# Optimization experiments

Hardware: AMD Instinct MI355X
Metric: run time of the kernel (lower is better)

## Reference

```python
import jax, jax.numpy as jnp
import numpy as np

NUM_CONTEXT = 8  # context panels; +1 choice -> 9 panels, 72 ordered pairs (i != j)

_PAIRS = np.array([(i, j) for i in range(9) for j in range(9) if i != j], dtype=np.int32)
I_IDX = jnp.asarray(_PAIRS[:, 0])  # [72]
J_IDX = jnp.asarray(_PAIRS[:, 1])  # [72]


def setup_inputs() -> dict:
    key = jax.random.key(0)
    ks = jax.random.split(key, 10)
    B, C, F, H = 256, 8, 512, 256
    s_in = 1.0 / np.sqrt(2 * F)
    s_h = 1.0 / np.sqrt(H)
    return {
        "context_features": jax.random.normal(ks[0], (B, NUM_CONTEXT, F), jnp.float32),
        "choice_features": jax.random.normal(ks[1], (B, C, F), jnp.float32),
        "W1": jax.random.uniform(ks[2], (2 * F, H), jnp.float32, -s_in, s_in),
        "b1": jax.random.uniform(ks[3], (H,), jnp.float32, -s_in, s_in),
        "W2": jax.random.uniform(ks[4], (H, H), jnp.float32, -s_h, s_h),
        "b2": jax.random.uniform(ks[5], (H,), jnp.float32, -s_h, s_h),
        "W3": jax.random.uniform(ks[6], (H, H), jnp.float32, -s_h, s_h),
        "b3": jax.random.uniform(ks[7], (H,), jnp.float32, -s_h, s_h),
        "W4": jax.random.uniform(ks[8], (H, 1), jnp.float32, -s_h, s_h),
        "b4": jax.random.uniform(ks[9], (1,), jnp.float32, -s_h, s_h),
    }


def reference(context_features, choice_features, W1, b1, W2, b2, W3, b3, W4, b4):
    B, C, F = choice_features.shape[0], choice_features.shape[1], choice_features.shape[2]
    # panels[b, c, p, f]: 8 context panels + 1 choice panel per candidate choice
    ctx = jnp.broadcast_to(context_features[:, None, :, :], (B, C, NUM_CONTEXT, F))
    panels = jnp.concatenate([ctx, choice_features[:, :, None, :]], axis=2)  # [B,C,9,F]
    # all 72 ordered pairs (i != j), concatenated features -> [B,C,72,2F]
    pair = jnp.concatenate([panels[:, :, I_IDX, :], panels[:, :, J_IDX, :]], axis=-1)
    # g_theta MLP
    h = jax.nn.relu(pair @ W1 + b1)
    h = jax.nn.relu(h @ W2 + b2)        # [B,C,72,H]
    agg = h.mean(axis=2)                # [B,C,H]
    # f_phi MLP (dropout is identity in eval mode)
    g = jax.nn.relu(agg @ W3 + b3)
    score = g @ W4 + b4                 # [B,C,1]
    return score[..., 0]                # [B,C]
```

## Files before the change

kernel.cpp:

```cpp
#include <hip/hip_runtime.h>
#include <hip/hip_bf16.h>


typedef __bf16 bf16_t;
typedef bf16_t bf16x8 __attribute__((ext_vector_type(8)));
typedef bf16_t bf16x4 __attribute__((ext_vector_type(4)));
typedef float f32x4 __attribute__((ext_vector_type(4)));

#define MFMA16(a, b, c) __builtin_amdgcn_mfma_f32_16x16x32_bf16((a), (b), (c), 0, 0, 0)

__global__ __launch_bounds__(256) void prep_kernel(
    const float* __restrict__ W1, const float* __restrict__ W2,
    const float* __restrict__ W3, bf16_t* __restrict__ Wp,
    bf16_t* __restrict__ W2T, bf16_t* __restrict__ W3T) {
  __shared__ float Ts[64][65];
  const int b = blockIdx.x;
  const int t = threadIdx.x;
  const int r = t >> 6;
  const int c = t & 63;
  const float* srcP;
  bf16_t* dstP;
  int srcRow, srcCol, dr0, dc0, dstride;
  if (b < 64) {
    const int k0 = (b >> 3) * 64, j0 = (b & 7) * 64;
    srcP = W1; dstP = Wp; dstride = 512;
    srcRow = (j0 < 256) ? k0 : 512 + k0;
    srcCol = (j0 < 256) ? j0 : j0 - 256;
    dr0 = j0; dc0 = k0;
  } else if (b < 80) {
    const int s = b - 64;
    const int k0 = (s >> 2) * 64, n0 = (s & 3) * 64;
    srcP = W2; dstP = W2T; dstride = 256;
    srcRow = k0; srcCol = n0; dr0 = n0; dc0 = k0;
  } else {
    const int s = b - 80;
    const int k0 = (s >> 2) * 64, n0 = (s & 3) * 64;
    srcP = W3; dstP = W3T; dstride = 256;
    srcRow = k0; srcCol = n0; dr0 = n0; dc0 = k0;
  }
  for (int i = 0; i < 16; ++i) {
    const int a = i * 4 + r;
    Ts[a][c] = srcP[(size_t)(srcRow + a) * 256 + srcCol + c];
  }
  __syncthreads();
  for (int i = 0; i < 16; ++i) {
    const int j = i * 4 + r;
    dstP[(size_t)(dr0 + j) * dstride + dc0 + c] = (bf16_t)Ts[c][j];
  }
}

__global__ __launch_bounds__(512) void k1_kernel(
    const float* __restrict__ ctx, const float* __restrict__ cho,
    const bf16_t* __restrict__ Wp, bf16_t* __restrict__ UV) {
  __shared__ bf16_t As[64][264];
  const int bm = blockIdx.x & 63;
  const int bn = blockIdx.x >> 6;
  const int t = threadIdx.x;
  const int lane = t & 63;
  const int w = t >> 6;
  const int col = lane & 15;
  const int quad = lane >> 4;
  const int n = bn * 128 + w * 16 + col;
  const int sr = t >> 3;
  const int gr = bm * 64 + sr;
  const int bi = gr >> 4;
  const int p = gr & 15;
  const float* src = (p < 8) ? ctx + (size_t)(bi * 8 + p) * 512
                             : cho + (size_t)(bi * 8 + (p - 8)) * 512;
  const int cb = (t & 7) * 4;
  f32x4 acc[4] = {};
  for (int half = 0; half < 2; ++half) {
    const int kbase = half * 256;
    for (int i = 0; i < 8; ++i) {
      const int c = cb + i * 32;
      const f32x4 x = *(const f32x4*)(src + kbase + c);
      bf16x4 y;
      for (int e = 0; e < 4; ++e) y[e] = (bf16_t)x[e];
      *(bf16x4*)(&As[sr][c]) = y;
    }
    __syncthreads();
    for (int ks = 0; ks < 8; ++ks) {
      const int k = ks * 32 + quad * 8;
      bf16x8 af[4];
      for (int mt = 0; mt < 4; ++mt)
        af[mt] = *(const bf16x8*)(&As[mt * 16 + col][k]);
      const bf16x8 bf = *(const bf16x8*)(Wp + (size_t)n * 512 + kbase + k);
      for (int mt = 0; mt < 4; ++mt) acc[mt] = MFMA16(af[mt], bf, acc[mt]);
    }
    __syncthreads();
  }
  for (int mt = 0; mt < 4; ++mt)
    for (int reg = 0; reg < 4; ++reg) {
      const int r = bm * 64 + mt * 16 + quad * 4 + reg;
      UV[(size_t)r * 512 + n] = (bf16_t)acc[mt][reg];
    }
}

__global__ __launch_bounds__(512) void k2_kernel(
    const bf16_t* __restrict__ UV, const float* __restrict__ b1,
    const float* __restrict__ b2, const bf16_t* __restrict__ W2T,
    const bf16_t* __restrict__ W3T, const float* __restrict__ b3,
    const float* __restrict__ W4, const float* __restrict__ b4,
    float* __restrict__ out) {
  __shared__ char smem[52224];
  bf16_t (*h1)[136] = (bf16_t(*)[136])smem;
  float (*S)[256] = (float(*)[256])smem;
  bf16_t (*Ag)[264] = (bf16_t(*)[264])(smem + 9216);
  float (*red)[8] = (float(*)[8])(smem + 9216 + 8448);
  const int b = blockIdx.x;
  const int t = threadIdx.x;
  const int lane = t & 63;
  const int w = t >> 6;
  const int col = lane & 15;
  const int quad = lane >> 4;
  const bf16_t* su = nullptr;
  const bf16_t* sv = nullptr;
  int sr = 0, sc0 = 0;
  if (t < 384) {
    sr = t >> 1;
    sc0 = (t & 1) * 64;
    if (sr < 56) {
      const int i = sr / 7;
      const int jj = sr - i * 7;
      const int j = jj + (jj >= i ? 1 : 0);
      su = UV + (size_t)(b * 16 + i) * 512;
      sv = UV + (size_t)(b * 16 + j) * 512 + 256;
    } else if (sr >= 64) {
      const int ch = (sr - 64) >> 4;
      const int rr = (sr - 64) & 15;
      if (rr < 8) {
        su = UV + (size_t)(b * 16 + 8 + ch) * 512;
        sv = UV + (size_t)(b * 16 + rr) * 512 + 256;
      } else {
        su = UV + (size_t)(b * 16 + (rr - 8)) * 512;
        sv = UV + (size_t)(b * 16 + 8 + ch) * 512 + 256;
      }
    }
  }
  const int mtb = (w & 1) * 6;
  const int q = w >> 1;
  f32x4 acc[6][4] = {};
  for (int half = 0; half < 2; ++half) {
    const int kbase = half * 128;
    if (t < 384) {
      if (su) {
        for (int c = sc0; c < sc0 + 64; c += 8) {
          const bf16x8 u8 = *(const bf16x8*)(su + kbase + c);
          const bf16x8 v8 = *(const bf16x8*)(sv + kbase + c);
          const f32x4 bb0 = *(const f32x4*)(b1 + kbase + c);
          const f32x4 bb1 = *(const f32x4*)(b1 + kbase + c + 4);
          bf16x8 y;
          for (int e = 0; e < 4; ++e)
            y[e] = (bf16_t)fmaxf((float)u8[e] + (float)v8[e] + bb0[e], 0.0f);
          for (int e = 0; e < 4; ++e)
            y[4 + e] = (bf16_t)fmaxf((float)u8[4 + e] + (float)v8[4 + e] + bb1[e], 0.0f);
          *(bf16x8*)(&h1[sr][c]) = y;
        }
      } else if (half == 0) {
        for (int c = sc0; c < sc0 + 64; c += 8)
          *(bf16x8*)(&h1[sr][c]) = (bf16x8)0.0f;
      }
    }
    __syncthreads();
    for (int ks = 0; ks < 4; ++ks) {
      const int k = ks * 32 + quad * 8;
      bf16x8 af[6], bf[4];
      for (int mt = 0; mt < 6; ++mt)
        af[mt] = *(const bf16x8*)(&h1[(mtb + mt) * 16 + col][k]);
      for (int nt = 0; nt < 4; ++nt) {
        const int n = q * 64 + nt * 16 + col;
        bf[nt] = *(const bf16x8*)(W2T + (size_t)n * 256 + kbase + k);
      }
      for (int mt = 0; mt < 6; ++mt)
        for (int nt = 0; nt < 4; ++nt)
          acc[mt][nt] = MFMA16(af[mt], bf[nt], acc[mt][nt]);
    }
    __syncthreads();
  }
  for (int nt = 0; nt < 4; ++nt) {
    const int n = q * 64 + nt * 16 + col;
    const float b2c = b2[n];
    float sctx = 0.0f;
    for (int mt = 0; mt < 6; ++mt) {
      const int gm = mtb + mt;
      float s = 0.0f;
      for (int reg = 0; reg < 4; ++reg) {
        const int row = gm * 16 + quad * 4 + reg;
        if (row < 56 || row >= 64) s += fmaxf(acc[mt][nt][reg] + b2c, 0.0f);
      }
      s += __shfl_xor(s, 16);
      s += __shfl_xor(s, 32);
      if (gm < 4) {
        sctx += s;
      } else if (lane < 16) {
        S[1 + (gm - 4)][n] = s;
      }
    }
    if (mtb == 0 && lane < 16) S[0][n] = sctx;
  }
  __syncthreads();
  {
    const int ch = t >> 6;
    const int n0 = (t & 63) * 4;
    bf16x4 y;
    for (int e = 0; e < 4; ++e)
      y[e] = (bf16_t)((S[0][n0 + e] + S[1 + ch][n0 + e]) * (1.0f / 72.0f));
    *(bf16x4*)(&Ag[ch][n0]) = y;
    *(bf16x4*)(&Ag[8 + ch][n0]) = (bf16x4)0.0f;
  }
  __syncthreads();
  f32x4 acc2[2] = {};
  for (int ks = 0; ks < 8; ++ks) {
    const int k = ks * 32 + quad * 8;
    const bf16x8 af = *(const bf16x8*)(&Ag[col][k]);
    for (int nt = 0; nt < 2; ++nt) {
      const int n = w * 32 + nt * 16 + col;
      const bf16x8 bf = *(const bf16x8*)(W3T + (size_t)n * 256 + k);
      acc2[nt] = MFMA16(af, bf, acc2[nt]);
    }
  }
  for (int reg = 0; reg < 4; ++reg) {
    float pr = 0.0f;
    for (int nt = 0; nt < 2; ++nt) {
      const int n = w * 32 + nt * 16 + col;
      pr += fmaxf(acc2[nt][reg] + b3[n], 0.0f) * W4[n];
    }
    pr += __shfl_xor(pr, 1);
    pr += __shfl_xor(pr, 2);
    pr += __shfl_xor(pr, 4);
    pr += __shfl_xor(pr, 8);
    if (col == 0 && quad < 2) red[w][quad * 4 + reg] = pr;
  }
  __syncthreads();
  if (t < 8) {
    float sc = b4[0];
    for (int ww = 0; ww < 8; ++ww) sc += red[ww][t];
    out[b * 8 + t] = sc;
  }
}

extern "C" void kernel_launch(void* const* d_in, const int* in_sizes, int n_in,
                              void* d_out, int out_size, void* d_ws, size_t ws_size,
                              hipStream_t stream) {
  (void)in_sizes; (void)n_in; (void)out_size; (void)ws_size;
  const float* ctx = (const float*)d_in[0];
  const float* cho = (const float*)d_in[1];
  const float* W1  = (const float*)d_in[2];
  const float* b1  = (const float*)d_in[3];
  const float* W2  = (const float*)d_in[4];
  const float* b2  = (const float*)d_in[5];
  const float* W3  = (const float*)d_in[6];
  const float* b3  = (const float*)d_in[7];
  const float* W4  = (const float*)d_in[8];
  const float* b4  = (const float*)d_in[9];
  char* ws = (char*)d_ws;
  bf16_t* Wp   = (bf16_t*)(ws + 0);
  bf16_t* W2T  = (bf16_t*)(ws + 524288);
  bf16_t* W3T  = (bf16_t*)(ws + 655360);
  bf16_t* UV   = (bf16_t*)(ws + 786432);
  float*  out  = (float*)d_out;

  prep_kernel<<<dim3(96), dim3(256), 0, stream>>>(W1, W2, W3, Wp, W2T, W3T);
  k1_kernel<<<dim3(256), dim3(512), 0, stream>>>(ctx, cho, Wp, UV);
  k2_kernel<<<dim3(256), dim3(512), 0, stream>>>(UV, b1, b2, W2T, W3T, b3, W4, b4, out);
}
```

Baseline: 109.7 us.

## Fuse first-layer projection into the pair MLP kernel, keeping UV in LDS

Merges the first GEMM kernel (per-panel U/V projections) into the second kernel. Each block now converts its 16 panels to bf16 in shared memory, computes the 16x512 UV tile with MFMA, and builds the pair hidden layer straight from LDS, so the global UV round trip and one launch disappear. The layer-2 GEMM now runs over all of K in one pass instead of two halves, which removes a sync pair. In exchange each block re-reads the full 512x512 Wp weight (256 blocks instead of 64 per column tile), and shared memory grows to about 118KB, allowing only one block per CU.

```diff
diff --git a/kernel.cpp b/kernel.cpp
--- a/kernel.cpp
+++ b/kernel.cpp
@@ -49,134 +49,118 @@
   }
 }
 
-__global__ __launch_bounds__(512) void k1_kernel(
+__global__ __launch_bounds__(512) void k2_kernel(
     const float* __restrict__ ctx, const float* __restrict__ cho,
-    const bf16_t* __restrict__ Wp, bf16_t* __restrict__ UV) {
-  __shared__ bf16_t As[64][264];
-  const int bm = blockIdx.x & 63;
-  const int bn = blockIdx.x >> 6;
-  const int t = threadIdx.x;
-  const int lane = t & 63;
-  const int w = t >> 6;
-  const int col = lane & 15;
-  const int quad = lane >> 4;
-  const int n = bn * 128 + w * 16 + col;
-  const int sr = t >> 3;
-  const int gr = bm * 64 + sr;
-  const int bi = gr >> 4;
-  const int p = gr & 15;
-  const float* src = (p < 8) ? ctx + (size_t)(bi * 8 + p) * 512
-                             : cho + (size_t)(bi * 8 + (p - 8)) * 512;
-  const int cb = (t & 7) * 4;
-  f32x4 acc[4] = {};
-  for (int half = 0; half < 2; ++half) {
-    const int kbase = half * 256;
-    for (int i = 0; i < 8; ++i) {
-      const int c = cb + i * 32;
-      const f32x4 x = *(const f32x4*)(src + kbase + c);
-      bf16x4 y;
-      for (int e = 0; e < 4; ++e) y[e] = (bf16_t)x[e];
-      *(bf16x4*)(&As[sr][c]) = y;
-    }
-    __syncthreads();
-    for (int ks = 0; ks < 8; ++ks) {
-      const int k = ks * 32 + quad * 8;
-      bf16x8 af[4];
-      for (int mt = 0; mt < 4; ++mt)
-        af[mt] = *(const bf16x8*)(&As[mt * 16 + col][k]);
-      const bf16x8 bf = *(const bf16x8*)(Wp + (size_t)n * 512 + kbase + k);
-      for (int mt = 0; mt < 4; ++mt) acc[mt] = MFMA16(af[mt], bf, acc[mt]);
-    }
-    __syncthreads();
-  }
-  for (int mt = 0; mt < 4; ++mt)
-    for (int reg = 0; reg < 4; ++reg) {
-      const int r = bm * 64 + mt * 16 + quad * 4 + reg;
-      UV[(size_t)r * 512 + n] = (bf16_t)acc[mt][reg];
-    }
-}
-
-__global__ __launch_bounds__(512) void k2_kernel(
-    const bf16_t* __restrict__ UV, const float* __restrict__ b1,
+    const bf16_t* __restrict__ Wp, const float* __restrict__ b1,
     const float* __restrict__ b2, const bf16_t* __restrict__ W2T,
     const bf16_t* __restrict__ W3T, const float* __restrict__ b3,
     const float* __restrict__ W4, const float* __restrict__ b4,
     float* __restrict__ out) {
-  __shared__ char smem[52224];
-  bf16_t (*h1)[136] = (bf16_t(*)[136])smem;
-  float (*S)[256] = (float(*)[256])smem;
-  bf16_t (*Ag)[264] = (bf16_t(*)[264])(smem + 9216);
-  float (*red)[8] = (float(*)[8])(smem + 9216 + 8448);
+  __shared__ char smem[118016];
+  bf16_t (*UVs)[520] = (bf16_t(*)[520])smem;
+  bf16_t (*Xs)[520]  = (bf16_t(*)[520])(smem + 16640);
+  bf16_t (*h1)[264]  = (bf16_t(*)[264])(smem + 16640);
+  float  (*S)[256]   = (float(*)[256])(smem + 16640);
+  bf16_t (*Ag)[264]  = (bf16_t(*)[264])(smem + 16640 + 9216);
+  float  (*red)[8]   = (float(*)[8])(smem + 16640 + 9216 + 8448);
   const int b = blockIdx.x;
   const int t = threadIdx.x;
   const int lane = t & 63;
   const int w = t >> 6;
   const int col = lane & 15;
   const int quad = lane >> 4;
-  const bf16_t* su = nullptr;
-  const bf16_t* sv = nullptr;
-  int sr = 0, sc0 = 0;
+
+  {
+    const int row = t >> 5;
+    const int c0 = (t & 31) * 16;
+    const float* src = (row < 8) ? ctx + ((size_t)b * 8 + row) * 512
+                                 : cho + ((size_t)b * 8 + (row - 8)) * 512;
+    const f32x4 x0 = *(const f32x4*)(src + c0);
+    const f32x4 x1 = *(const f32x4*)(src + c0 + 4);
+    const f32x4 x2 = *(const f32x4*)(src + c0 + 8);
+    const f32x4 x3 = *(const f32x4*)(src + c0 + 12);
+    bf16x8 y0, y1;
+    for (int e = 0; e < 4; ++e) { y0[e] = (bf16_t)x0[e]; y0[4 + e] = (bf16_t)x1[e]; }
+    for (int e = 0; e < 4; ++e) { y1[e] = (bf16_t)x2[e]; y1[4 + e] = (bf16_t)x3[e]; }
+    *(bf16x8*)(&Xs[row][c0]) = y0;
+    *(bf16x8*)(&Xs[row][c0 + 8]) = y1;
+  }
+  __syncthreads();
+
+  {
+    f32x4 acc1[4] = {};
+    for (int ks = 0; ks < 16; ++ks) {
+      const int k = ks * 32 + quad * 8;
+      const bf16x8 af = *(const bf16x8*)(&Xs[col][k]);
+      for (int nt = 0; nt < 4; ++nt) {
+        const int n = w * 64 + nt * 16 + col;
+        const bf16x8 bfr = *(const bf16x8*)(Wp + (size_t)n * 512 + k);
+        acc1[nt] = MFMA16(af, bfr, acc1[nt]);
+      }
+    }
+    for (int nt = 0; nt < 4; ++nt) {
+      const int n = w * 64 + nt * 16 + col;
+      for (int reg = 0; reg < 4; ++reg)
+        UVs[quad * 4 + reg][n] = (bf16_t)acc1[nt][reg];
+    }
+  }
+  __syncthreads();
+
   if (t < 384) {
-    sr = t >> 1;
-    sc0 = (t & 1) * 64;
+    const int sr = t >> 1;
+    const int sc0 = (t & 1) * 128;
+    const bf16_t* su = nullptr;
+    const bf16_t* sv = nullptr;
     if (sr < 56) {
       const int i = sr / 7;
       const int jj = sr - i * 7;
       const int j = jj + (jj >= i ? 1 : 0);
-      su = UV + (size_t)(b * 16 + i) * 512;
-      sv = UV + (size_t)(b * 16 + j) * 512 + 256;
+      su = UVs[i];
+      sv = UVs[j] + 256;
     } else if (sr >= 64) {
       const int ch = (sr - 64) >> 4;
       const int rr = (sr - 64) & 15;
-      if (rr < 8) {
-        su = UV + (size_t)(b * 16 + 8 + ch) * 512;
-        sv = UV + (size_t)(b * 16 + rr) * 512 + 256;
-      } else {
-        su = UV + (size_t)(b * 16 + (rr - 8)) * 512;
-        sv = UV + (size_t)(b * 16 + 8 + ch) * 512 + 256;
-      }
-    }
-  }
+      if (rr < 8) { su = UVs[8 + ch]; sv = UVs[rr] + 256; }
+      else        { su = UVs[rr - 8]; sv = UVs[8 + ch] + 256; }
+    }
+    if (su) {
+      for (int c = sc0; c < sc0 + 128; c += 8) {
+        const bf16x8 u8 = *(const bf16x8*)(su + c);
+        const bf16x8 v8 = *(const bf16x8*)(sv + c);
+        const f32x4 bb0 = *(const f32x4*)(b1 + c);
+        const f32x4 bb1 = *(const f32x4*)(b1 + c + 4);
+        bf16x8 y;
+        for (int e = 0; e < 4; ++e)
+          y[e] = (bf16_t)fmaxf((float)u8[e] + (float)v8[e] + bb0[e], 0.0f);
+        for (int e = 0; e < 4; ++e)
+          y[4 + e] = (bf16_t)fmaxf((float)u8[4 + e] + (float)v8[4 + e] + bb1[e], 0.0f);
+        *(bf16x8*)(&h1[sr][c]) = y;
+      }
+    } else {
+      for (int c = sc0; c < sc0 + 128; c += 8)
+        *(bf16x8*)(&h1[sr][c]) = (bf16x8)0.0f;
+    }
+  }
+  __syncthreads();
+
   const int mtb = (w & 1) * 6;
   const int q = w >> 1;
   f32x4 acc[6][4] = {};
-  for (int half = 0; half < 2; ++half) {
-    const int kbase = half * 128;
-    if (t < 384) {
-      if (su) {
-        for (int c = sc0; c < sc0 + 64; c += 8) {
-          const bf16x8 u8 = *(const bf16x8*)(su + kbase + c);
-          const bf16x8 v8 = *(const bf16x8*)(sv + kbase + c);
-          const f32x4 bb0 = *(const f32x4*)(b1 + kbase + c);
-          const f32x4 bb1 = *(const f32x4*)(b1 + kbase + c + 4);
-          bf16x8 y;
-          for (int e = 0; e < 4; ++e)
-            y[e] = (bf16_t)fmaxf((float)u8[e] + (float)v8[e] + bb0[e], 0.0f);
-          for (int e = 0; e < 4; ++e)
-            y[4 + e] = (bf16_t)fmaxf((float)u8[4 + e] + (float)v8[4 + e] + bb1[e], 0.0f);
-          *(bf16x8*)(&h1[sr][c]) = y;
-        }
-      } else if (half == 0) {
-        for (int c = sc0; c < sc0 + 64; c += 8)
-          *(bf16x8*)(&h1[sr][c]) = (bf16x8)0.0f;
-      }
-    }
-    __syncthreads();
-    for (int ks = 0; ks < 4; ++ks) {
-      const int k = ks * 32 + quad * 8;
-      bf16x8 af[6], bf[4];
-      for (int mt = 0; mt < 6; ++mt)
-        af[mt] = *(const bf16x8*)(&h1[(mtb + mt) * 16 + col][k]);
-      for (int nt = 0; nt < 4; ++nt) {
-        const int n = q * 64 + nt * 16 + col;
-        bf[nt] = *(const bf16x8*)(W2T + (size_t)n * 256 + kbase + k);
-      }
-      for (int mt = 0; mt < 6; ++mt)
-        for (int nt = 0; nt < 4; ++nt)
-          acc[mt][nt] = MFMA16(af[mt], bf[nt], acc[mt][nt]);
-    }
-    __syncthreads();
-  }
+  for (int ks = 0; ks < 8; ++ks) {
+    const int k = ks * 32 + quad * 8;
+    bf16x8 af[6], bfr[4];
+    for (int mt = 0; mt < 6; ++mt)
+      af[mt] = *(const bf16x8*)(&h1[(mtb + mt) * 16 + col][k]);
+    for (int nt = 0; nt < 4; ++nt) {
+      const int n = q * 64 + nt * 16 + col;
+      bfr[nt] = *(const bf16x8*)(W2T + (size_t)n * 256 + k);
+    }
+    for (int mt = 0; mt < 6; ++mt)
+      for (int nt = 0; nt < 4; ++nt)
+        acc[mt][nt] = MFMA16(af[mt], bfr[nt], acc[mt][nt]);
+  }
+  __syncthreads();
+
   for (int nt = 0; nt < 4; ++nt) {
     const int n = q * 64 + nt * 16 + col;
     const float b2c = b2[n];
@@ -215,8 +199,8 @@
     const bf16x8 af = *(const bf16x8*)(&Ag[col][k]);
     for (int nt = 0; nt < 2; ++nt) {
       const int n = w * 32 + nt * 16 + col;
-      const bf16x8 bf = *(const bf16x8*)(W3T + (size_t)n * 256 + k);
-      acc2[nt] = MFMA16(af, bf, acc2[nt]);
+      const bf16x8 bfr = *(const bf16x8*)(W3T + (size_t)n * 256 + k);
+      acc2[nt] = MFMA16(af, bfr, acc2[nt]);
     }
   }
   for (int reg = 0; reg < 4; ++reg) {
@@ -257,10 +241,9 @@
   bf16_t* Wp   = (bf16_t*)(ws + 0);
   bf16_t* W2T  = (bf16_t*)(ws + 524288);
   bf16_t* W3T  = (bf16_t*)(ws + 655360);
-  bf16_t* UV   = (bf16_t*)(ws + 786432);
   float*  out  = (float*)d_out;
 
   prep_kernel<<<dim3(96), dim3(256), 0, stream>>>(W1, W2, W3, Wp, W2T, W3T);
-  k1_kernel<<<dim3(256), dim3(512), 0, stream>>>(ctx, cho, Wp, UV);
-  k2_kernel<<<dim3(256), dim3(512), 0, stream>>>(UV, b1, b2, W2T, W3T, b3, W4, b4, out);
+  k2_kernel<<<dim3(256), dim3(512), 0, stream>>>(ctx, cho, Wp, b1, b2, W2T, W3T,
+                                                 b3, W4, b4, out);
 }
```

Result: no change. 110.9 us (+1.1%).
